# Kernel tuning notes

Hardware: AMD Instinct MI355X
Metric: run time of the kernel (lower is better)

Reference implementation:

```python
import jax, jax.numpy as jnp
import numpy as np

# Architecture constants (from init_kwargs / ActionConfig)
R = 4          # vae_time_compression_ratio
WS = 2         # windows_size
PAD_T = R * WS # preprocessor left-padding
HID = 512      # action hidden_size
KD_IN = 16     # keyboard_dim_in (movement feature dim)
C_IMG = 3072   # img_hidden_size
KH = 1024      # keyboard_hidden_dim
NH = 16        # heads_num
HD = 64        # keyboard_head_dim
EPS = 1e-6


def setup_inputs() -> dict:
    key = jax.random.key(0)
    ks = jax.random.split(key, 8)
    B, T, Hs, Ws, NF = 1, 3, 44, 80, 81
    S = Hs * Ws

    def w(k, shape, s=0.02):
        return jax.random.normal(k, shape, jnp.float32) * s

    return {
        "x": jax.random.normal(ks[0], (B, T * S, C_IMG), jnp.float32),
        "condition": jax.random.normal(ks[1], (B, NF, KD_IN), jnp.float32),
        "me_w1": w(ks[2], (KD_IN, HID)), "me_b1": jnp.zeros((HID,), jnp.float32),
        "me_w2": w(ks[3], (HID, HID)), "me_b2": jnp.zeros((HID,), jnp.float32),
        "q_w": w(ks[4], (C_IMG, KH)), "q_b": jnp.zeros((KH,), jnp.float32),
        "kv_w": w(ks[5], (HID * WS * R, 2 * KH)), "kv_b": jnp.zeros((2 * KH,), jnp.float32),
        "qn_w": jnp.ones((HD,), jnp.float32), "kn_w": jnp.ones((HD,), jnp.float32),
        "out_w": w(ks[6], (KH, C_IMG)), "out_b": jnp.zeros((C_IMG,), jnp.float32),
        "H": Hs, "W": Ws, "T": T, "num_frame_per_block": T,
    }


def _rmsnorm(x, w):
    return x * jax.lax.rsqrt(jnp.mean(x * x, axis=-1, keepdims=True) + EPS) * w


def _preprocess(condition, me_w1, me_b1, me_w2, me_b2, num_frame_per_block):
    # MovementPreprocessor.forward with is_causal=True
    B, NF, _ = condition.shape
    pad = jnp.broadcast_to(condition[:, :1, :], (B, PAD_T, condition.shape[-1]))
    cp = jnp.concatenate([pad, condition], axis=1)            # [B, PAD_T+NF, KD_IN]
    emb = jax.nn.silu(cp @ me_w1 + me_b1) @ me_w2 + me_b2     # [B, PAD_T+NF, HID]
    n_feats = (NF - 1) // R + 1
    start = R * (n_feats - num_frame_per_block - WS) + PAD_T  # python int (static)
    emb = emb[:, start:, :]
    # vectorized replacement of the python-loop window slicing+stack
    win = jnp.arange(num_frame_per_block)[:, None] * R + jnp.arange(WS * R)[None, :]
    gm = emb[:, win, :]                                       # [B, L, WS*R, HID]
    return gm.reshape(B, num_frame_per_block, WS * R * HID)   # [B, L, 4096]


def reference(x, condition, me_w1, me_b1, me_w2, me_b2, q_w, q_b, kv_w, kv_b,
              qn_w, kn_w, out_w, out_b, H, W, T, num_frame_per_block):
    B = x.shape[0]
    S = H * W
    L = num_frame_per_block

    mf = _preprocess(condition, me_w1, me_b1, me_w2, me_b2, L)  # [B, L, HID*WS*R]

    # q: [B, T*S, C_IMG] -> [B, S, T, h, d]
    q = (x @ q_w + q_b).reshape(B, T, S, NH, HD).transpose(0, 2, 1, 3, 4)

    # k, v: [B, L, h, d] (NOT expanded over S; broadcast inside attention instead)
    kv = (mf @ kv_w + kv_b).reshape(B, L, 2, NH, HD)
    k, v = kv[:, :, 0], kv[:, :, 1]

    q = _rmsnorm(q, qn_w)
    k = _rmsnorm(k, kn_w)

    scale = 1.0 / np.sqrt(HD).astype(np.float32)
    scores = jnp.einsum('bsthd,blhd->bshtl', q, k) * scale      # [B,S,h,T,L]
    attn = jax.nn.softmax(scores, axis=-1)
    o = jnp.einsum('bshtl,blhd->bsthd', attn, v)                # [B,S,T,h,d]

    # '(B S) T H D -> B (T S) (H D)'
    o = o.transpose(0, 2, 1, 3, 4).reshape(B, T * S, NH * HD)
    return x + (o @ out_w + out_b)
```

## Files before the change

kernel.cpp:

```cpp
#include <hip/hip_runtime.h>

#define TOK  10560
#define CIMG 3072
#define KHD  1024

typedef unsigned short ushort_t;
typedef unsigned int u32;
using bf16x8 = __attribute__((ext_vector_type(8))) __bf16;
using f32x4  = __attribute__((ext_vector_type(4))) float;

#define GLD_LDS16(gp, lp) __builtin_amdgcn_global_load_lds( \
    (const __attribute__((address_space(1))) u32*)(gp), \
    (__attribute__((address_space(3))) u32*)(lp), 16, 0, 0)

static __device__ __forceinline__ unsigned short f2bf(float f){
  union { float f; unsigned u; } x; x.f = f;
  unsigned r = x.u + 0x7fffu + ((x.u >> 16) & 1u);
  return (unsigned short)(r >> 16);
}
static __device__ __forceinline__ float wave_sum(float v){
  #pragma unroll
  for (int off = 32; off > 0; off >>= 1) v += __shfl_xor(v, off, 64);
  return v;
}

__global__ __launch_bounds__(256) void k_pre1(const float* __restrict__ cond,
    const float* __restrict__ w1, const float* __restrict__ b1,
    float* __restrict__ h1){
  __shared__ float cs[16][16];
  int t = threadIdx.x;
  if (t < 256) cs[t >> 4][t & 15] = cond[(64 + (t >> 4)) * 16 + (t & 15)];
  __syncthreads();
  #pragma unroll
  for (int i = 0; i < 4; ++i){
    int idx = blockIdx.x * 256 + t + i * 2048;
    int r = idx >> 9, c = idx & 511;
    float s = b1[c];
    #pragma unroll
    for (int j = 0; j < 16; ++j) s += cs[r][j] * w1[j * 512 + c];
    h1[idx] = s / (1.f + __expf(-s));
  }
}

__global__ __launch_bounds__(256) void k_pre2(const float* __restrict__ h1,
    const float* __restrict__ w2, const float* __restrict__ b2,
    float* __restrict__ emb){
  int idx = blockIdx.x * 256 + threadIdx.x;
  int r = idx >> 9, c = idx & 511;
  const float* hp = h1 + r * 512;
  const float* wp = w2 + c;
  float acc = b2[c];
  #pragma unroll 8
  for (int j = 0; j < 512; ++j) acc += hp[j] * wp[(size_t)j * 512];
  emb[idx] = acc;
}

__global__ __launch_bounds__(256) void k_kv(const float* __restrict__ emb,
                                            const float* __restrict__ kvw,
                                            float* __restrict__ part){
  int bl = blockIdx.x;
  int l = bl / 128, rem = bl % 128, nt = rem / 16, kc = rem % 16;
  int n = nt * 256 + threadIdx.x;
  const float* e = emb + 2048 * l + kc * 256;
  const float* w = kvw + (size_t)(kc * 256) * 2048 + n;
  float acc = 0.f;
  for (int r = 0; r < 256; ++r) acc += e[r] * w[(size_t)r * 2048];
  part[kc * 6144 + l * 2048 + n] = acc;
}

__global__ void k_knorm(const float* __restrict__ part, const float* __restrict__ kvb,
                        const float* __restrict__ knw, float* __restrict__ kn,
                        float* __restrict__ vv){
  int wid = threadIdx.x >> 6, lane = threadIdx.x & 63;
  for (int i = 0; i < 12; ++i){
    int g = wid * 12 + i;
    int l = g >> 4, h = g & 15;
    int ik = l * 2048 + h * 64 + lane;
    float kk = kvb[h * 64 + lane];
    float v  = kvb[1024 + h * 64 + lane];
    for (int p = 0; p < 16; ++p){ kk += part[p * 6144 + ik]; v += part[p * 6144 + ik + 1024]; }
    float ss = wave_sum(kk * kk);
    kn[l * 1024 + h * 64 + lane] = kk * rsqrtf(ss * (1.f/64.f) + 1e-6f) * knw[lane];
    vv[l * 1024 + h * 64 + lane] = v;
  }
}

__global__ __launch_bounds__(256) void k_tconv(const float* __restrict__ src,
                                               ushort_t* __restrict__ dst,
                                               int R, int C){
  __shared__ float tile[32][33];
  int nTr = R >> 5;
  int tr = blockIdx.x % nTr, tc = blockIdx.x / nTr;
  int r0 = tr * 32, c0 = tc * 32, t = threadIdx.x;
  #pragma unroll
  for (int i = 0; i < 4; ++i){
    int idx = t + i * 256; int r = idx >> 5, c = idx & 31;
    tile[r][c] = src[(size_t)(r0 + r) * C + c0 + c];
  }
  __syncthreads();
  #pragma unroll
  for (int i = 0; i < 4; ++i){
    int idx = t + i * 256; int rr = idx >> 5, cc = idx & 31;
    dst[(size_t)(c0 + rr) * R + r0 + cc] = f2bf(tile[cc][rr]);
  }
}

__global__ __launch_bounds__(256) void k_xconv(const float* __restrict__ x,
                                               ushort_t* __restrict__ xb, int n4){
  for (int i = blockIdx.x * 256 + threadIdx.x; i < n4; i += gridDim.x * 256){
    float4 v = ((const float4*)x)[i];
    ushort4 o;
    o.x = f2bf(v.x); o.y = f2bf(v.y); o.z = f2bf(v.z); o.w = f2bf(v.w);
    ((ushort4*)xb)[i] = o;
  }
}

__global__ __launch_bounds__(512, 4) void gemm_fused(
    const ushort_t* __restrict__ A, const ushort_t* __restrict__ Bt,
    const float* __restrict__ bias, const float* __restrict__ kn,
    const float* __restrict__ qnw, float* __restrict__ acoef){
  __shared__ __align__(16) unsigned char lds[81920];
  const int tid = threadIdx.x;
  const int lane = tid & 63, wid = tid >> 6;
  const int wm = wid >> 1, wn = wid & 1;
  const int l15 = lane & 15, kg = lane >> 4;

  int bid = blockIdx.x;
  bid = (bid & 7) * 55 + (bid >> 3);
  const int mt = bid >> 3, nt = bid & 7;
  const int mbase = mt * 192, nbase = nt << 7;

  const int sr  = tid >> 1;
  const int skh = (tid & 1) ^ ((sr >> 2) & 1);
  const ushort_t* gA = A + (size_t)(mbase + sr) * CIMG + skh * 8;
  const int u   = tid - 384;
  const int skb = (u & 1) ^ ((u >> 3) & 1);
  const ushort_t* gB0 = Bt + (size_t)(nbase + (u >> 1)) * CIMG + skb * 8;
  const ushort_t* gB1 = gB0 + (size_t)64 * CIMG;

  auto stage = [&](int t, int c, int b){
    const int gk = t * 64 + c * 16;
    if (wid < 6){
      unsigned char* dst = lds + b * 40960 + c * 6144 + wid * 1024;
      GLD_LDS16(gA + gk, dst);
    } else {
      unsigned char* dst = lds + b * 40960 + 24576 + c * 4096 + (wid - 6) * 1024;
      GLD_LDS16(gB0 + gk, dst);
      GLD_LDS16(gB1 + gk, dst + 2048);
    }
  };
#define WAITC2 { if (wid < 6) asm volatile("s_waitcnt vmcnt(2)" ::: "memory"); \
                 else         asm volatile("s_waitcnt vmcnt(4)" ::: "memory"); }

  const int arl = wm * 48 + l15;
  const int brl = wn * 64 + l15;
  const int kh  = ((kg & 1) ^ ((l15 >> 2) & 1)) * 16;
  const unsigned aBase = (unsigned)((kg >> 1) * 6144 + arl * 32 + kh);
  const unsigned bBase = (unsigned)(24576 + (kg >> 1) * 4096 + brl * 32 + kh);

  f32x4 acc[3][4];
  #pragma unroll
  for (int m = 0; m < 3; ++m)
    #pragma unroll
    for (int n = 0; n < 4; ++n) acc[m][n] = {0.f, 0.f, 0.f, 0.f};

  bf16x8 afr[3], bfr[4];

#define PH_READ(base, KSL) { _Pragma("unroll") \
    for (int n = 0; n < 4; ++n) \
      bfr[n] = *(const bf16x8*)((base) + bBase + (KSL)*8192 + n*512); \
    _Pragma("unroll") \
    for (int m = 0; m < 3; ++m) \
      afr[m] = *(const bf16x8*)((base) + aBase + (KSL)*12288 + m*512); }
#define PH_MFMA { __builtin_amdgcn_s_setprio(1); _Pragma("unroll") \
    for (int m = 0; m < 3; ++m){ _Pragma("unroll") \
      for (int n = 0; n < 4; ++n) \
        acc[m][n] = __builtin_amdgcn_mfma_f32_16x16x32_bf16(afr[m], bfr[n], acc[m][n], 0, 0, 0); } \
    __builtin_amdgcn_s_setprio(0); }

  const int T = CIMG / 64;

  stage(0, 0, 0); stage(0, 1, 0); stage(0, 2, 0); stage(0, 3, 0);
  WAITC2;
  __builtin_amdgcn_s_barrier();

  for (int t = 0; t < T - 1; ++t){
    const int b = t & 1;
    const unsigned char* base = lds + b * 40960;
    PH_READ(base, 0);
    stage(t + 1, 0, b ^ 1); stage(t + 1, 1, b ^ 1);
    WAITC2;
    __builtin_amdgcn_s_barrier();
    PH_MFMA;
    __builtin_amdgcn_s_barrier();
    PH_READ(base, 1);
    stage(t + 1, 2, b ^ 1); stage(t + 1, 3, b ^ 1);
    WAITC2;
    __builtin_amdgcn_s_barrier();
    PH_MFMA;
    __builtin_amdgcn_s_barrier();
  }
  {
    const unsigned char* base = lds + ((T - 1) & 1) * 40960;
    PH_READ(base, 0);
    asm volatile("s_waitcnt vmcnt(0)" ::: "memory");
    __builtin_amdgcn_s_barrier();
    PH_MFMA;
    __builtin_amdgcn_s_barrier();
    PH_READ(base, 1);
    PH_MFMA;
  }
#undef PH_READ
#undef PH_MFMA
#undef WAITC2

  const int hglob = nt * 2 + wn;
  float qnwv[4], qbv[4], knv0[4], knv1[4], knv2[4];
  #pragma unroll
  for (int n = 0; n < 4; ++n){
    int d = n * 16 + l15;
    qnwv[n] = qnw[d];
    qbv[n]  = bias[nbase + wn * 64 + d];
    knv0[n] = kn[hglob * 64 + d];
    knv1[n] = kn[1024 + hglob * 64 + d];
    knv2[n] = kn[2048 + hglob * 64 + d];
  }
  #pragma unroll
  for (int m = 0; m < 3; ++m){
    #pragma unroll
    for (int j = 0; j < 4; ++j){
      float q[4], ssq = 0.f;
      #pragma unroll
      for (int n = 0; n < 4; ++n){ q[n] = acc[m][n][j] + qbv[n]; ssq += q[n] * q[n]; }
      #pragma unroll
      for (int off = 1; off < 16; off <<= 1) ssq += __shfl_xor(ssq, off, 64);
      float rs = rsqrtf(ssq * (1.f/64.f) + 1e-6f);
      float s0 = 0.f, s1 = 0.f, s2 = 0.f;
      #pragma unroll
      for (int n = 0; n < 4; ++n){
        float qn = q[n] * rs * qnwv[n];
        s0 += qn * knv0[n]; s1 += qn * knv1[n]; s2 += qn * knv2[n];
      }
      #pragma unroll
      for (int off = 1; off < 16; off <<= 1){
        s0 += __shfl_xor(s0, off, 64);
        s1 += __shfl_xor(s1, off, 64);
        s2 += __shfl_xor(s2, off, 64);
      }
      s0 *= 0.125f; s1 *= 0.125f; s2 *= 0.125f;
      float mx = fmaxf(s0, fmaxf(s1, s2));
      float e0 = __expf(s0 - mx), e1 = __expf(s1 - mx), e2 = __expf(s2 - mx);
      float inv = 1.f / (e0 + e1 + e2);
      int grow = mbase + wm * 48 + m * 16 + kg * 4 + j;
      if (l15 == 0){
        float2 a12 = {e1 * inv, e2 * inv};
        *(float2*)(acoef + (size_t)grow * 32 + hglob * 2) = a12;
      }
    }
  }
}

__global__ __launch_bounds__(512) void k_uv(const float* __restrict__ vv,
    const float* __restrict__ ow, float* __restrict__ U){
  int b = blockIdx.x;
  int i = b / 6, cc = b % 6;
  int h = i / 3, l = i % 3;
  int c = cc * 512 + threadIdx.x;
  const float* vp = vv + l * 1024 + h * 64;
  const float* wp = ow + (size_t)(h * 64) * 3072 + c;
  float acc = 0.f;
  #pragma unroll
  for (int d = 0; d < 64; ++d) acc += vp[d] * wp[(size_t)d * 3072];
  U[(size_t)i * 3072 + c] = acc;
}

__global__ __launch_bounds__(256) void k_ubase(const float* __restrict__ U,
    const float* __restrict__ ob, float* __restrict__ base, float* __restrict__ D){
  int c = blockIdx.x * 256 + threadIdx.x;
  float b = ob[c];
  #pragma unroll
  for (int h = 0; h < 16; ++h){
    float u0 = U[(size_t)(h * 3 + 0) * 3072 + c];
    float u1 = U[(size_t)(h * 3 + 1) * 3072 + c];
    float u2 = U[(size_t)(h * 3 + 2) * 3072 + c];
    b += u0;
    D[(size_t)(h * 2 + 0) * 3072 + c] = u1 - u0;
    D[(size_t)(h * 2 + 1) * 3072 + c] = u2 - u0;
  }
  base[c] = b;
}

__global__ __launch_bounds__(256) void k_rank32v(const float* __restrict__ x,
    const float* __restrict__ acoef, const float* __restrict__ D,
    const float* __restrict__ base, float* __restrict__ out){
  __shared__ __align__(16) float as[8][32];
  const int tid = threadIdx.x;
  const int rb = blockIdx.x / 3, cc = blockIdx.x % 3;
  const int r0 = rb * 8;
  const int c  = cc * 1024 + tid * 4;

  if (tid < 256) ((float*)as)[tid] = acoef[(size_t)r0 * 32 + tid];
  __syncthreads();

  f32x4 accv[8];
  #pragma unroll
  for (int r = 0; r < 8; ++r) accv[r] = {0.f, 0.f, 0.f, 0.f};

  #pragma unroll 4
  for (int k = 0; k < 32; ++k){
    f32x4 d4 = *(const f32x4*)(D + (size_t)k * 3072 + c);
    #pragma unroll
    for (int r = 0; r < 8; ++r){
      float a = as[r][k];
      accv[r][0] += a * d4[0]; accv[r][1] += a * d4[1];
      accv[r][2] += a * d4[2]; accv[r][3] += a * d4[3];
    }
  }

  f32x4 b4 = *(const f32x4*)(base + c);
  #pragma unroll
  for (int r = 0; r < 8; ++r){
    const size_t o = (size_t)(r0 + r) * 3072 + c;
    f32x4 xv = *(const f32x4*)(x + o);
    f32x4 ov;
    ov[0] = xv[0] + b4[0] + accv[r][0];
    ov[1] = xv[1] + b4[1] + accv[r][1];
    ov[2] = xv[2] + b4[2] + accv[r][2];
    ov[3] = xv[3] + b4[3] + accv[r][3];
    *(f32x4*)(out + o) = ov;
  }
}

extern "C" void kernel_launch(void* const* d_in, const int* in_sizes, int n_in,
                              void* d_out, int out_size, void* d_ws, size_t ws_size,
                              hipStream_t stream){
  const float* x    = (const float*)d_in[0];
  const float* cond = (const float*)d_in[1];
  const float* mew1 = (const float*)d_in[2];
  const float* meb1 = (const float*)d_in[3];
  const float* mew2 = (const float*)d_in[4];
  const float* meb2 = (const float*)d_in[5];
  const float* qw   = (const float*)d_in[6];
  const float* qb   = (const float*)d_in[7];
  const float* kvw  = (const float*)d_in[8];
  const float* kvb  = (const float*)d_in[9];
  const float* qnw  = (const float*)d_in[10];
  const float* knw  = (const float*)d_in[11];
  const float* ow   = (const float*)d_in[12];
  const float* ob   = (const float*)d_in[13];

  char* ws = (char*)d_ws;
  float*    emb    = (float*)(ws + 0);
  float*    kvpart = (float*)(ws + 32768);
  float*    kn     = (float*)(ws + 425984);
  float*    vv     = (float*)(ws + 438272);
  ushort_t* qwt    = (ushort_t*)(ws + 450560);
  float*    U      = (float*)(ws + 6742016);
  float*    base   = (float*)(ws + 7331840);
  float*    Dbuf   = (float*)(ws + 7344128);
  float*    acoef  = (float*)(ws + 7737344);
  float*    h1buf  = (float*)(ws + 9089024);

  ushort_t* xb = (ushort_t*)d_out;

  k_pre1<<<8, 256, 0, stream>>>(cond, mew1, meb1, h1buf);
  k_pre2<<<32, 256, 0, stream>>>(h1buf, mew2, meb2, emb);
  k_kv<<<384, 256, 0, stream>>>(emb, kvw, kvpart);
  k_knorm<<<1, 256, 0, stream>>>(kvpart, kvb, knw, kn, vv);
  k_uv<<<288, 512, 0, stream>>>(vv, ow, U);
  k_ubase<<<12, 256, 0, stream>>>(U, ob, base, Dbuf);
  k_tconv<<<3072, 256, 0, stream>>>(qw, qwt, 3072, 1024);
  k_xconv<<<2048, 256, 0, stream>>>(x, xb, (TOK * CIMG) / 4);
  gemm_fused<<<440, 512, 0, stream>>>(xb, qwt, qb, kn, qnw, acoef);
  k_rank32v<<<3960, 256, 0, stream>>>(x, acoef, Dbuf, base, (float*)d_out);
}
```

Before: 292.1 us.

## Fuse fp32-to-bf16 conversion of x into GEMM A-operand register loads

Removes the separate k_xconv pass that wrote a bf16 copy of x, and has the GEMM read fp32 x straight from global memory into registers. It converts them with v_cvt_pk_bf16_f32 just before the MFMA. Only the B operand is still staged through LDS, so LDS drops to 32KB and the barrier/pipeline schedule is rebuilt around register double-buffering of A. This saves a full read and write pass over x, but each GEMM tile now reads fp32 A, which is twice the bytes, directly from global memory. Those reads are repeated across the 8 N-tiles without LDS sharing between waves.

```diff
diff --git a/kernel.cpp b/kernel.cpp
--- a/kernel.cpp
+++ b/kernel.cpp
@@ -17,6 +17,10 @@
   union { float f; unsigned u; } x; x.f = f;
   unsigned r = x.u + 0x7fffu + ((x.u >> 16) & 1u);
   return (unsigned short)(r >> 16);
+}
+static __device__ __forceinline__ u32 cvtpk(float a, float b){
+  u32 r; asm("v_cvt_pk_bf16_f32 %0, %1, %2" : "=v"(r) : "v"(a), "v"(b));
+  return r;
 }
 static __device__ __forceinline__ float wave_sum(float v){
   #pragma unroll
@@ -105,21 +109,11 @@
   }
 }
 
-__global__ __launch_bounds__(256) void k_xconv(const float* __restrict__ x,
-                                               ushort_t* __restrict__ xb, int n4){
-  for (int i = blockIdx.x * 256 + threadIdx.x; i < n4; i += gridDim.x * 256){
-    float4 v = ((const float4*)x)[i];
-    ushort4 o;
-    o.x = f2bf(v.x); o.y = f2bf(v.y); o.z = f2bf(v.z); o.w = f2bf(v.w);
-    ((ushort4*)xb)[i] = o;
-  }
-}
-
 __global__ __launch_bounds__(512, 4) void gemm_fused(
-    const ushort_t* __restrict__ A, const ushort_t* __restrict__ Bt,
+    const float* __restrict__ A, const ushort_t* __restrict__ Bt,
     const float* __restrict__ bias, const float* __restrict__ kn,
     const float* __restrict__ qnw, float* __restrict__ acoef){
-  __shared__ __align__(16) unsigned char lds[81920];
+  __shared__ __align__(16) unsigned char lds[32768];
   const int tid = threadIdx.x;
   const int lane = tid & 63, wid = tid >> 6;
   const int wm = wid >> 1, wn = wid & 1;
@@ -130,33 +124,25 @@
   const int mt = bid >> 3, nt = bid & 7;
   const int mbase = mt * 192, nbase = nt << 7;
 
-  const int sr  = tid >> 1;
-  const int skh = (tid & 1) ^ ((sr >> 2) & 1);
-  const ushort_t* gA = A + (size_t)(mbase + sr) * CIMG + skh * 8;
-  const int u   = tid - 384;
-  const int skb = (u & 1) ^ ((u >> 3) & 1);
-  const ushort_t* gB0 = Bt + (size_t)(nbase + (u >> 1)) * CIMG + skb * 8;
-  const ushort_t* gB1 = gB0 + (size_t)64 * CIMG;
-
-  auto stage = [&](int t, int c, int b){
-    const int gk = t * 64 + c * 16;
-    if (wid < 6){
-      unsigned char* dst = lds + b * 40960 + c * 6144 + wid * 1024;
-      GLD_LDS16(gA + gk, dst);
-    } else {
-      unsigned char* dst = lds + b * 40960 + 24576 + c * 4096 + (wid - 6) * 1024;
-      GLD_LDS16(gB0 + gk, dst);
-      GLD_LDS16(gB1 + gk, dst + 2048);
-    }
-  };
-#define WAITC2 { if (wid < 6) asm volatile("s_waitcnt vmcnt(2)" ::: "memory"); \
-                 else         asm volatile("s_waitcnt vmcnt(4)" ::: "memory"); }
-
-  const int arl = wm * 48 + l15;
+  const float* Af = A + (size_t)(mbase + wm * 48 + l15) * CIMG;
+
+  const int skb = (lane & 1) ^ ((lane >> 3) & 1);
+  const ushort_t* gB0; const ushort_t* gB1;
+  unsigned char* dB0; unsigned char* dB1;
+  {
+    int s0 = wid * 2, c0_ = s0 >> 2, sub0 = s0 & 3;
+    int s1 = wid * 2 + 1, c1_ = s1 >> 2, sub1 = s1 & 3;
+    gB0 = Bt + (size_t)(nbase + sub0 * 32 + (lane >> 1)) * CIMG + c0_ * 16 + skb * 8;
+    gB1 = Bt + (size_t)(nbase + sub1 * 32 + (lane >> 1)) * CIMG + c1_ * 16 + skb * 8;
+    dB0 = lds + c0_ * 4096 + sub0 * 1024;
+    dB1 = lds + c1_ * 4096 + sub1 * 1024;
+  }
+#define STAGE_B0(tt) GLD_LDS16(gB0 + (size_t)(tt) * 64, dB0 + (((tt) & 1) << 14))
+#define STAGE_B1(tt) GLD_LDS16(gB1 + (size_t)(tt) * 64, dB1 + (((tt) & 1) << 14))
+
   const int brl = wn * 64 + l15;
   const int kh  = ((kg & 1) ^ ((l15 >> 2) & 1)) * 16;
-  const unsigned aBase = (unsigned)((kg >> 1) * 6144 + arl * 32 + kh);
-  const unsigned bBase = (unsigned)(24576 + (kg >> 1) * 4096 + brl * 32 + kh);
+  const unsigned bBase = (unsigned)((kg >> 1) * 4096 + brl * 32 + kh);
 
   f32x4 acc[3][4];
   #pragma unroll
@@ -164,55 +150,71 @@
     #pragma unroll
     for (int n = 0; n < 4; ++n) acc[m][n] = {0.f, 0.f, 0.f, 0.f};
 
-  bf16x8 afr[3], bfr[4];
-
-#define PH_READ(base, KSL) { _Pragma("unroll") \
-    for (int n = 0; n < 4; ++n) \
-      bfr[n] = *(const bf16x8*)((base) + bBase + (KSL)*8192 + n*512); \
+  f32x4 A0[6], A1[6];
+
+#define ALOAD(dst, tt, ss) { \
+    const int koff = (tt) * 64 + (ss) * 32 + kg * 8; \
     _Pragma("unroll") \
-    for (int m = 0; m < 3; ++m) \
-      afr[m] = *(const bf16x8*)((base) + aBase + (KSL)*12288 + m*512); }
-#define PH_MFMA { __builtin_amdgcn_s_setprio(1); _Pragma("unroll") \
-    for (int m = 0; m < 3; ++m){ _Pragma("unroll") \
-      for (int n = 0; n < 4; ++n) \
-        acc[m][n] = __builtin_amdgcn_mfma_f32_16x16x32_bf16(afr[m], bfr[n], acc[m][n], 0, 0, 0); } \
+    for (int m = 0; m < 3; ++m){ \
+      dst[2*m]   = *(const f32x4*)(Af + (size_t)m * (16 * CIMG) + koff); \
+      dst[2*m+1] = *(const f32x4*)(Af + (size_t)m * (16 * CIMG) + koff + 4); } }
+
+#define DO_HALF(Aset, rbase, S_) { \
+    const unsigned char* _rb = (rbase); \
+    bf16x8 b0 = *(const bf16x8*)(_rb + bBase + (S_)*8192 + 0*512); \
+    bf16x8 b1 = *(const bf16x8*)(_rb + bBase + (S_)*8192 + 1*512); \
+    bf16x8 b2 = *(const bf16x8*)(_rb + bBase + (S_)*8192 + 2*512); \
+    bf16x8 b3 = *(const bf16x8*)(_rb + bBase + (S_)*8192 + 3*512); \
+    __builtin_amdgcn_s_setprio(1); \
+    _Pragma("unroll") \
+    for (int m = 0; m < 3; ++m){ \
+      union { u32 u[4]; bf16x8 v; } _c; \
+      _c.u[0] = cvtpk(Aset[2*m][0],   Aset[2*m][1]); \
+      _c.u[1] = cvtpk(Aset[2*m][2],   Aset[2*m][3]); \
+      _c.u[2] = cvtpk(Aset[2*m+1][0], Aset[2*m+1][1]); \
+      _c.u[3] = cvtpk(Aset[2*m+1][2], Aset[2*m+1][3]); \
+      acc[m][0] = __builtin_amdgcn_mfma_f32_16x16x32_bf16(_c.v, b0, acc[m][0], 0, 0, 0); \
+      acc[m][1] = __builtin_amdgcn_mfma_f32_16x16x32_bf16(_c.v, b1, acc[m][1], 0, 0, 0); \
+      acc[m][2] = __builtin_amdgcn_mfma_f32_16x16x32_bf16(_c.v, b2, acc[m][2], 0, 0, 0); \
+      acc[m][3] = __builtin_amdgcn_mfma_f32_16x16x32_bf16(_c.v, b3, acc[m][3], 0, 0, 0); \
+    } \
     __builtin_amdgcn_s_setprio(0); }
 
   const int T = CIMG / 64;
 
-  stage(0, 0, 0); stage(0, 1, 0); stage(0, 2, 0); stage(0, 3, 0);
-  WAITC2;
+  ALOAD(A0, 0, 0);
+  STAGE_B0(0); STAGE_B1(0);
+  asm volatile("s_waitcnt vmcnt(0)" ::: "memory");
   __builtin_amdgcn_s_barrier();
+  asm volatile("" ::: "memory");
 
   for (int t = 0; t < T - 1; ++t){
-    const int b = t & 1;
-    const unsigned char* base = lds + b * 40960;
-    PH_READ(base, 0);
-    stage(t + 1, 0, b ^ 1); stage(t + 1, 1, b ^ 1);
-    WAITC2;
+    const unsigned char* rb = lds + ((t & 1) << 14);
+    ALOAD(A1, t, 1);
+    asm volatile("s_waitcnt vmcnt(6)" ::: "memory");
     __builtin_amdgcn_s_barrier();
-    PH_MFMA;
+    asm volatile("" ::: "memory");
+    STAGE_B0(t + 1);
+    DO_HALF(A0, rb, 0);
+    ALOAD(A0, t + 1, 0);
+    asm volatile("s_waitcnt vmcnt(7)" ::: "memory");
+    STAGE_B1(t + 1);
+    DO_HALF(A1, rb, 1);
+  }
+  {
+    const unsigned char* rb = lds + (((T - 1) & 1) << 14);
+    ALOAD(A1, T - 1, 1);
+    asm volatile("s_waitcnt vmcnt(6)" ::: "memory");
     __builtin_amdgcn_s_barrier();
-    PH_READ(base, 1);
-    stage(t + 1, 2, b ^ 1); stage(t + 1, 3, b ^ 1);
-    WAITC2;
-    __builtin_amdgcn_s_barrier();
-    PH_MFMA;
-    __builtin_amdgcn_s_barrier();
-  }
-  {
-    const unsigned char* base = lds + ((T - 1) & 1) * 40960;
-    PH_READ(base, 0);
+    asm volatile("" ::: "memory");
+    DO_HALF(A0, rb, 0);
     asm volatile("s_waitcnt vmcnt(0)" ::: "memory");
-    __builtin_amdgcn_s_barrier();
-    PH_MFMA;
-    __builtin_amdgcn_s_barrier();
-    PH_READ(base, 1);
-    PH_MFMA;
-  }
-#undef PH_READ
-#undef PH_MFMA
-#undef WAITC2
+    DO_HALF(A1, rb, 1);
+  }
+#undef ALOAD
+#undef DO_HALF
+#undef STAGE_B0
+#undef STAGE_B1
 
   const int hglob = nt * 2 + wn;
   float qnwv[4], qbv[4], knv0[4], knv1[4], knv2[4];
@@ -361,8 +363,6 @@
   float*    acoef  = (float*)(ws + 7737344);
   float*    h1buf  = (float*)(ws + 9089024);
 
-  ushort_t* xb = (ushort_t*)d_out;
-
   k_pre1<<<8, 256, 0, stream>>>(cond, mew1, meb1, h1buf);
   k_pre2<<<32, 256, 0, stream>>>(h1buf, mew2, meb2, emb);
   k_kv<<<384, 256, 0, stream>>>(emb, kvw, kvpart);
@@ -370,7 +370,6 @@
   k_uv<<<288, 512, 0, stream>>>(vv, ow, U);
   k_ubase<<<12, 256, 0, stream>>>(U, ob, base, Dbuf);
   k_tconv<<<3072, 256, 0, stream>>>(qw, qwt, 3072, 1024);
-  k_xconv<<<2048, 256, 0, stream>>>(x, xb, (TOK * CIMG) / 4);
-  gemm_fused<<<440, 512, 0, stream>>>(xb, qwt, qb, kn, qnw, acoef);
+  gemm_fused<<<440, 512, 0, stream>>>(x, qwt, qb, kn, qnw, acoef);
   k_rank32v<<<3960, 256, 0, stream>>>(x, acoef, Dbuf, base, (float*)d_out);
 }
```

Result: slower. 435.5 us (+49.1%).
